# Kernel tuning notes

Hardware: AMD Instinct MI355X
Metric: run time of the kernel (lower is better)

## Reference

```python
import jax, jax.numpy as jnp
import numpy as np

N, E, G = 30000, 480000, 64
IN, H, L = 24, 512, 6


def setup_inputs() -> dict:
    key = jax.random.key(0)
    ks = jax.random.split(key, 20)
    s = 0.05
    inp = {
        "x": jax.random.normal(ks[0], (N, IN), dtype=jnp.float32),
        "edge_index": jax.random.randint(ks[1], (2, E), 0, N, dtype=jnp.int64),
        "batch": jnp.sort(jax.random.randint(ks[2], (N,), 0, G, dtype=jnp.int64)),
        # node encoder
        "enc_w": jax.random.normal(ks[3], (IN, H), dtype=jnp.float32) * s,
        "enc_b": jnp.zeros((H,), dtype=jnp.float32),
        # per-layer message MLP (stacked over L layers), weights stored [in, out]
        "mlp_w1": jax.random.normal(ks[4], (L, H, H), dtype=jnp.float32) * s,
        "mlp_b1": jnp.zeros((L, H), dtype=jnp.float32),
        "mlp_w2": jax.random.normal(ks[5], (L, H, H), dtype=jnp.float32) * s,
        "mlp_b2": jnp.zeros((L, H), dtype=jnp.float32),
        # per-layer GRUCell params, [in, 3H] layout (gates order: r, z, n)
        "gru_wih": jax.random.normal(ks[6], (L, H, 3 * H), dtype=jnp.float32) * s,
        "gru_whh": jax.random.normal(ks[7], (L, H, 3 * H), dtype=jnp.float32) * s,
        "gru_bih": jnp.zeros((L, 3 * H), dtype=jnp.float32),
        "gru_bhh": jnp.zeros((L, 3 * H), dtype=jnp.float32),
        # head MLP
        "head_w1": jax.random.normal(ks[8], (H, H // 2), dtype=jnp.float32) * s,
        "head_b1": jnp.zeros((H // 2,), dtype=jnp.float32),
        "head_w2": jax.random.normal(ks[9], (H // 2, 1), dtype=jnp.float32) * s,
        "head_b2": jnp.zeros((1,), dtype=jnp.float32),
    }
    return inp


def _forward(x, edge_index, batch, enc_w, enc_b, mlp_w1, mlp_b1, mlp_w2, mlp_b2,
             gru_wih, gru_whh, gru_bih, gru_bhh, head_w1, head_b1, head_w2, head_b2):
    src, dst = edge_index[0], edge_index[1]
    h = x @ enc_w + enc_b  # [N, H]
    for l in range(L):
        # message MLP depends only on x_j, so compute per-node then gather
        msg = jnp.maximum(h @ mlp_w1[l] + mlp_b1[l], 0.0) @ mlp_w2[l] + mlp_b2[l]  # [N, H]
        # scatter-add over edges + self-loop contribution (add_self_loops)
        m = jax.ops.segment_sum(msg[src], dst, num_segments=N) + msg  # [N, H]
        # GRUCell(input=m, hidden=h); torch gate order: reset, update, new
        gi = m @ gru_wih[l] + gru_bih[l]
        gh = h @ gru_whh[l] + gru_bhh[l]
        r = jax.nn.sigmoid(gi[:, :H] + gh[:, :H])
        z = jax.nn.sigmoid(gi[:, H:2 * H] + gh[:, H:2 * H])
        n = jnp.tanh(gi[:, 2 * H:] + r * gh[:, 2 * H:])
        h = (1.0 - z) * n + z * h
    # global mean pool per graph
    sums = jax.ops.segment_sum(h, batch, num_segments=G)
    cnt = jax.ops.segment_sum(jnp.ones((N,), dtype=h.dtype), batch, num_segments=G)
    pooled = sums / jnp.maximum(cnt, 1.0)[:, None]  # [G, H]
    out = jnp.maximum(pooled @ head_w1 + head_b1, 0.0) @ head_w2 + head_b2
    return out[:, 0]  # [G]


def reference(x, edge_index, batch, enc_w, enc_b, mlp_w1, mlp_b1, mlp_w2, mlp_b2,
              gru_wih, gru_whh, gru_bih, gru_bhh, head_w1, head_b1, head_w2, head_b2):
    return _forward(x, edge_index, batch, enc_w, enc_b, mlp_w1, mlp_b1, mlp_w2, mlp_b2,
                    gru_wih, gru_whh, gru_bih, gru_bhh, head_w1, head_b1, head_w2, head_b2)
```

## Files before the change

kernel.cpp:

```cpp
#include <hip/hip_runtime.h>
#include <hip/hip_bf16.h>
#include <math.h>

#define N_NODES 30000
#define N_EDGES 480000
#define N_GRAPH 64
#define DIN 24
#define HD 512
#define NL 6

typedef __hip_bfloat16 bf16;
using short8 = __attribute__((ext_vector_type(8))) short;
using f32x4 = __attribute__((ext_vector_type(4))) float;

#define ASYNC16(gp, lp)                                              \
    __builtin_amdgcn_global_load_lds(                                \
        (const __attribute__((address_space(1))) void*)(gp),         \
        (__attribute__((address_space(3))) void*)(lp), 16, 0, 0)

__device__ __forceinline__ float sigmoidf_(float x) { return 1.0f / (1.0f + expf(-x)); }
__device__ __forceinline__ float b2f(unsigned short u) {
    return __uint_as_float(((unsigned int)u) << 16);
}
__device__ __forceinline__ unsigned short f2b(float f) {
    bf16 b = __float2bfloat16(f);
    return *(unsigned short*)&b;
}

__global__ __launch_bounds__(256) void enc_kernel(const float* __restrict__ x,
                                                  const float* __restrict__ w,
                                                  const float* __restrict__ b,
                                                  bf16* __restrict__ h) {
    __shared__ float xs[DIN];
    int row = blockIdx.x;
    int tid = threadIdx.x;
    if (tid < DIN) xs[tid] = x[row * DIN + tid];
    __syncthreads();
    for (int c = tid; c < HD; c += 256) {
        float acc = b[c];
#pragma unroll
        for (int k = 0; k < DIN; k++) acc = fmaf(xs[k], w[k * HD + c], acc);
        h[(size_t)row * HD + c] = __float2bfloat16(acc);
    }
}

__global__ __launch_bounds__(256) void twcvt_kernel(const float* __restrict__ W,
                                                    bf16* __restrict__ WtH,
                                                    bf16* __restrict__ WtL, int Nc) {
    __shared__ float s[32][33];
    int l = blockIdx.z;
    const float* Wp = W + (size_t)l * HD * Nc;
    size_t ob = (size_t)l * HD * Nc;
    int k0 = blockIdx.y * 32, c0 = blockIdx.x * 32;
    int tx = threadIdx.x & 31, ty = threadIdx.x >> 5;
    for (int r = ty; r < 32; r += 8) s[r][tx] = Wp[(size_t)(k0 + r) * Nc + c0 + tx];
    __syncthreads();
    for (int r = ty; r < 32; r += 8) {
        float v = s[tx][r];
        unsigned short hu = f2b(v);
        float hf = b2f(hu);
        size_t o = ob + (size_t)(c0 + r) * HD + k0 + tx;
        *(unsigned short*)&WtH[o] = hu;
        WtL[o] = __float2bfloat16(v - hf);
    }
}

template <bool RELU>
__global__ __launch_bounds__(256) void gemm_mfma(const bf16* __restrict__ A,
                                                 const bf16* __restrict__ WtH,
                                                 const bf16* __restrict__ WtL,
                                                 const float* __restrict__ bias,
                                                 bf16* __restrict__ C, int n) {
    __shared__ bf16 As[128 * 32];
    __shared__ bf16 BH[128 * 32];
    __shared__ bf16 BL[128 * 32];
    int tid = threadIdx.x;
    int wv = tid >> 6, lane = tid & 63;
    int quad = lane >> 4, l16 = lane & 15;
    int crow = lane >> 2, cseg = lane & 3;
    int gseg = cseg ^ ((crow >> 1) & 3);
    int fsw = (quad ^ ((l16 >> 1) & 3)) * 8;
    int row0 = blockIdx.y * 128, col0 = blockIdx.x * 128;
    f32x4 acc[2][8] = {};

    int aoff[4], alds[4];
    int boff[8];
    const bf16* wb = (wv == 2) ? WtH : WtL;
    bf16* bdst = (wv == 2) ? BH : BL;
    if (wv < 2) {
#pragma unroll
        for (int j = 0; j < 4; j++) {
            int ch = wv * 4 + j;
            int gr = row0 + ch * 16 + crow;
            if (gr > n - 1) gr = n - 1;
            aoff[j] = gr * HD + gseg * 8;
            alds[j] = ch * 512;
        }
    } else {
#pragma unroll
        for (int s = 0; s < 8; s++) boff[s] = (col0 + s * 16 + crow) * HD + gseg * 8;
    }

    for (int kt = 0; kt < 512; kt += 32) {
        if (wv < 2) {
#pragma unroll
            for (int j = 0; j < 4; j++) ASYNC16(&A[aoff[j] + kt], &As[alds[j]]);
        } else {
#pragma unroll
            for (int s = 0; s < 8; s++) ASYNC16(&wb[boff[s] + kt], &bdst[s * 512]);
        }
        __syncthreads();
        short8 bfr[2][2];
#pragma unroll
        for (int t = 0; t < 2; t++) {
            int fo = ((wv * 2 + t) * 16 + l16) * 32 + fsw;
            bfr[t][0] = *(const short8*)&BH[fo];
            bfr[t][1] = *(const short8*)&BL[fo];
        }
#pragma unroll
        for (int i = 0; i < 8; i++) {
            short8 af = *(const short8*)&As[(i * 16 + l16) * 32 + fsw];
#pragma unroll
            for (int t = 0; t < 2; t++) {
                acc[t][i] = __builtin_amdgcn_mfma_f32_16x16x32_bf16(af, bfr[t][0], acc[t][i], 0, 0, 0);
                acc[t][i] = __builtin_amdgcn_mfma_f32_16x16x32_bf16(af, bfr[t][1], acc[t][i], 0, 0, 0);
            }
        }
        __syncthreads();
    }
#pragma unroll
    for (int t = 0; t < 2; t++) {
        int col = col0 + (wv * 2 + t) * 16 + l16;
        float bb = bias[col];
#pragma unroll
        for (int i = 0; i < 8; i++) {
#pragma unroll
            for (int r = 0; r < 4; r++) {
                int row = row0 + i * 16 + quad * 4 + r;
                if (row < n) {
                    float v = acc[t][i][r] + bb;
                    if (RELU) v = fmaxf(v, 0.0f);
                    C[(size_t)row * HD + col] = __float2bfloat16(v);
                }
            }
        }
    }
}

__global__ __launch_bounds__(256, 2) void gru_mfma(const bf16* __restrict__ M,
                                                   const bf16* __restrict__ Hc,
                                                   const bf16* __restrict__ WiH,
                                                   const bf16* __restrict__ WiL,
                                                   const bf16* __restrict__ WhH,
                                                   const bf16* __restrict__ WhL,
                                                   const float* __restrict__ bih,
                                                   const float* __restrict__ bhh,
                                                   bf16* __restrict__ Hn, int n) {
    __shared__ bf16 Ms[128 * 32];
    __shared__ bf16 Hs[128 * 32];
    __shared__ bf16 Ws[12 * 64 * 32];
    int tid = threadIdx.x;
    int wv = tid >> 6, lane = tid & 63;
    int quad = lane >> 4, l16 = lane & 15;
    int crow = lane >> 2, cseg = lane & 3;
    int gseg = cseg ^ ((crow >> 1) & 3);
    int fsw = (quad ^ ((l16 >> 1) & 3)) * 8;
    int row0 = blockIdx.y * 128, col0 = blockIdx.x * 64;
    f32x4 aR[8] = {}, aZ[8] = {}, aI[8] = {}, aHn[8] = {};

    int moff[8];
    const bf16* wgp[4];
    int wlds[4];
    if (wv == 0) {
#pragma unroll
        for (int j = 0; j < 8; j++) {
            int gr = row0 + j * 16 + crow;
            if (gr > n - 1) gr = n - 1;
            moff[j] = gr * HD + gseg * 8;
        }
    } else {
        const bf16* wbase[4] = {WiH, WiL, WhH, WhL};
#pragma unroll
        for (int pp = 0; pp < 4; pp++) {
            int p = (wv - 1) * 4 + pp;
            int mat = (p >= 6);
            int q = p - mat * 6;
            int g = q >> 1, pl = q & 1;
            const bf16* base = wbase[mat * 2 + pl] + (size_t)(g * HD + col0) * HD;
            wgp[pp] = base + crow * HD + gseg * 8;
            wlds[pp] = p * 2048;
        }
    }

    for (int kt = 0; kt < 512; kt += 32) {
        if (wv == 0) {
#pragma unroll
            for (int j = 0; j < 8; j++) {
                ASYNC16(&M[moff[j] + kt], &Ms[j * 512]);
                ASYNC16(&Hc[moff[j] + kt], &Hs[j * 512]);
            }
        } else {
#pragma unroll
            for (int pp = 0; pp < 4; pp++)
#pragma unroll
                for (int s = 0; s < 4; s++)
                    ASYNC16(wgp[pp] + (size_t)s * 16 * HD + kt, &Ws[wlds[pp] + s * 512]);
        }
        __syncthreads();
        int fo = (wv * 16 + l16) * 32 + fsw;
        short8 wrh = *(const short8*)&Ws[0 * 2048 + fo];
        short8 wrl = *(const short8*)&Ws[1 * 2048 + fo];
        short8 wzh = *(const short8*)&Ws[2 * 2048 + fo];
        short8 wzl = *(const short8*)&Ws[3 * 2048 + fo];
        short8 wnh = *(const short8*)&Ws[4 * 2048 + fo];
        short8 wnl = *(const short8*)&Ws[5 * 2048 + fo];
        short8 vrh = *(const short8*)&Ws[6 * 2048 + fo];
        short8 vrl = *(const short8*)&Ws[7 * 2048 + fo];
        short8 vzh = *(const short8*)&Ws[8 * 2048 + fo];
        short8 vzl = *(const short8*)&Ws[9 * 2048 + fo];
        short8 vnh = *(const short8*)&Ws[10 * 2048 + fo];
        short8 vnl = *(const short8*)&Ws[11 * 2048 + fo];
#pragma unroll
        for (int i = 0; i < 8; i++) {
            short8 am = *(const short8*)&Ms[(i * 16 + l16) * 32 + fsw];
            short8 ah = *(const short8*)&Hs[(i * 16 + l16) * 32 + fsw];
            aR[i] = __builtin_amdgcn_mfma_f32_16x16x32_bf16(am, wrh, aR[i], 0, 0, 0);
            aR[i] = __builtin_amdgcn_mfma_f32_16x16x32_bf16(am, wrl, aR[i], 0, 0, 0);
            aR[i] = __builtin_amdgcn_mfma_f32_16x16x32_bf16(ah, vrh, aR[i], 0, 0, 0);
            aR[i] = __builtin_amdgcn_mfma_f32_16x16x32_bf16(ah, vrl, aR[i], 0, 0, 0);
            aZ[i] = __builtin_amdgcn_mfma_f32_16x16x32_bf16(am, wzh, aZ[i], 0, 0, 0);
            aZ[i] = __builtin_amdgcn_mfma_f32_16x16x32_bf16(am, wzl, aZ[i], 0, 0, 0);
            aZ[i] = __builtin_amdgcn_mfma_f32_16x16x32_bf16(ah, vzh, aZ[i], 0, 0, 0);
            aZ[i] = __builtin_amdgcn_mfma_f32_16x16x32_bf16(ah, vzl, aZ[i], 0, 0, 0);
            aI[i] = __builtin_amdgcn_mfma_f32_16x16x32_bf16(am, wnh, aI[i], 0, 0, 0);
            aI[i] = __builtin_amdgcn_mfma_f32_16x16x32_bf16(am, wnl, aI[i], 0, 0, 0);
            aHn[i] = __builtin_amdgcn_mfma_f32_16x16x32_bf16(ah, vnh, aHn[i], 0, 0, 0);
            aHn[i] = __builtin_amdgcn_mfma_f32_16x16x32_bf16(ah, vnl, aHn[i], 0, 0, 0);
        }
        __syncthreads();
    }
    const unsigned short* hp = (const unsigned short*)Hc;
    int col = col0 + wv * 16 + l16;
    float brz = bih[col] + bhh[col];
    float bzz = bih[HD + col] + bhh[HD + col];
    float bin_ = bih[2 * HD + col];
    float bhn_ = bhh[2 * HD + col];
#pragma unroll
    for (int i = 0; i < 8; i++) {
#pragma unroll
        for (int r = 0; r < 4; r++) {
            int row = row0 + i * 16 + quad * 4 + r;
            if (row < n) {
                float rg = sigmoidf_(aR[i][r] + brz);
                float zg = sigmoidf_(aZ[i][r] + bzz);
                float ng = tanhf(aI[i][r] + bin_ + rg * (aHn[i][r] + bhn_));
                float hold = b2f(hp[(size_t)row * HD + col]);
                Hn[(size_t)row * HD + col] = __float2bfloat16((1.0f - zg) * ng + zg * hold);
            }
        }
    }
}

__global__ __launch_bounds__(256) void deg_kernel(const int* __restrict__ dst,
                                                  int* __restrict__ deg) {
    int e = blockIdx.x * 256 + threadIdx.x;
    if (e < N_EDGES) atomicAdd(&deg[dst[e]], 1);
}

__global__ __launch_bounds__(1024) void scan_kernel(const int* __restrict__ deg,
                                                    int* __restrict__ offs) {
    __shared__ int buf[1024];
    __shared__ int carry_s;
    int tid = threadIdx.x;
    if (tid == 0) carry_s = 0;
    __syncthreads();
    for (int base = 0; base < N_NODES; base += 1024) {
        int v = (base + tid < N_NODES) ? deg[base + tid] : 0;
        buf[tid] = v;
        __syncthreads();
        for (int s = 1; s < 1024; s <<= 1) {
            int t = (tid >= s) ? buf[tid - s] : 0;
            __syncthreads();
            buf[tid] += t;
            __syncthreads();
        }
        int incl = buf[tid];
        if (base + tid < N_NODES) offs[base + tid] = carry_s + incl - v;
        __syncthreads();
        if (tid == 0) carry_s += buf[1023];
        __syncthreads();
    }
    if (tid == 0) offs[N_NODES] = carry_s;
}

__global__ __launch_bounds__(256) void bucket_kernel(const int* __restrict__ src,
                                                     const int* __restrict__ dst,
                                                     const int* __restrict__ offs,
                                                     int* __restrict__ cursor,
                                                     unsigned short* __restrict__ elist) {
    int e = blockIdx.x * 256 + threadIdx.x;
    if (e >= N_EDGES) return;
    int d = dst[e];
    int pos = atomicAdd(&cursor[d], 1);
    elist[offs[d] + pos] = (unsigned short)src[e];
}

__global__ __launch_bounds__(256) void gather_kernel(const bf16* __restrict__ msg,
                                                     bf16* __restrict__ m,
                                                     const unsigned short* __restrict__ elist,
                                                     const int* __restrict__ offs) {
    int nid = blockIdx.x, tid = threadIdx.x;
    int beg = offs[nid], end = offs[nid + 1];
    const unsigned int* mp = (const unsigned int*)msg;
    unsigned int u = mp[(size_t)nid * 256 + tid];
    float ax = b2f((unsigned short)(u & 0xffffu));
    float ay = b2f((unsigned short)(u >> 16));
    int e = beg;
    for (; e + 3 < end; e += 4) {
        unsigned int v0 = mp[(size_t)elist[e] * 256 + tid];
        unsigned int v1 = mp[(size_t)elist[e + 1] * 256 + tid];
        unsigned int v2 = mp[(size_t)elist[e + 2] * 256 + tid];
        unsigned int v3 = mp[(size_t)elist[e + 3] * 256 + tid];
        ax += b2f((unsigned short)(v0 & 0xffffu)) + b2f((unsigned short)(v1 & 0xffffu)) +
              b2f((unsigned short)(v2 & 0xffffu)) + b2f((unsigned short)(v3 & 0xffffu));
        ay += b2f((unsigned short)(v0 >> 16)) + b2f((unsigned short)(v1 >> 16)) +
              b2f((unsigned short)(v2 >> 16)) + b2f((unsigned short)(v3 >> 16));
    }
    for (; e < end; e++) {
        unsigned int v0 = mp[(size_t)elist[e] * 256 + tid];
        ax += b2f((unsigned short)(v0 & 0xffffu));
        ay += b2f((unsigned short)(v0 >> 16));
    }
    unsigned int out = ((unsigned int)f2b(ay) << 16) | (unsigned int)f2b(ax);
    ((unsigned int*)m)[(size_t)nid * 256 + tid] = out;
}

__global__ __launch_bounds__(256) void pool_kernel(const bf16* __restrict__ h,
                                                   const int* __restrict__ batch,
                                                   float* __restrict__ pooled,
                                                   float* __restrict__ cnt) {
    int g = blockIdx.x;
    int col = blockIdx.y * 256 + threadIdx.x;
    int lo = 0, hi = N_NODES;
    while (lo < hi) { int mid = (lo + hi) >> 1; if (batch[mid] < g) lo = mid + 1; else hi = mid; }
    int gs = lo;
    hi = N_NODES;
    while (lo < hi) { int mid = (lo + hi) >> 1; if (batch[mid] < g + 1) lo = mid + 1; else hi = mid; }
    int ge = lo;
    const unsigned short* hp = (const unsigned short*)h;
    float acc = 0.0f;
    int r = gs;
    for (; r + 3 < ge; r += 4) {
        acc += b2f(hp[(size_t)r * HD + col]) + b2f(hp[(size_t)(r + 1) * HD + col]) +
               b2f(hp[(size_t)(r + 2) * HD + col]) + b2f(hp[(size_t)(r + 3) * HD + col]);
    }
    for (; r < ge; r++) acc += b2f(hp[(size_t)r * HD + col]);
    pooled[g * HD + col] = acc;
    if (blockIdx.y == 0 && threadIdx.x == 0) cnt[g] = (float)(ge - gs);
}

__global__ __launch_bounds__(256) void head_kernel(const float* __restrict__ pooled,
                                                   const float* __restrict__ cnt,
                                                   const float* __restrict__ w1,
                                                   const float* __restrict__ b1,
                                                   const float* __restrict__ w2,
                                                   const float* __restrict__ b2,
                                                   float* __restrict__ out) {
    __shared__ float prow[HD];
    __shared__ float red[256];
    int g = blockIdx.x, tid = threadIdx.x;
    float c = fmaxf(cnt[g], 1.0f);
    for (int j = tid; j < HD; j += 256) prow[j] = pooled[g * HD + j] / c;
    __syncthreads();
    float acc = b1[tid];
    for (int k = 0; k < HD; k++) acc = fmaf(prow[k], w1[k * 256 + tid], acc);
    red[tid] = fmaxf(acc, 0.0f) * w2[tid];
    __syncthreads();
    for (int s = 128; s > 0; s >>= 1) {
        if (tid < s) red[tid] += red[tid + s];
        __syncthreads();
    }
    if (tid == 0) out[g] = red[0] + b2[0];
}

extern "C" void kernel_launch(void* const* d_in, const int* in_sizes, int n_in,
                              void* d_out, int out_size, void* d_ws, size_t ws_size,
                              hipStream_t stream) {
    const float* x = (const float*)d_in[0];
    const int* eidx = (const int*)d_in[1];
    const int* batch = (const int*)d_in[2];
    const float* enc_w = (const float*)d_in[3];
    const float* enc_b = (const float*)d_in[4];
    const float* mlp_w1 = (const float*)d_in[5];
    const float* mlp_b1 = (const float*)d_in[6];
    const float* mlp_w2 = (const float*)d_in[7];
    const float* mlp_b2 = (const float*)d_in[8];
    const float* gru_wih = (const float*)d_in[9];
    const float* gru_whh = (const float*)d_in[10];
    const float* gru_bih = (const float*)d_in[11];
    const float* gru_bhh = (const float*)d_in[12];
    const float* head_w1 = (const float*)d_in[13];
    const float* head_b1 = (const float*)d_in[14];
    const float* head_w2 = (const float*)d_in[15];
    const float* head_b2 = (const float*)d_in[16];
    const int* src = eidx;
    const int* dst = eidx + N_EDGES;

    const size_t NH = (size_t)N_NODES * HD;
    char* p = (char*)d_ws;
    auto alloc = [&](size_t bytes) { char* q = p; p += (bytes + 255) & ~(size_t)255; return q; };
    bf16* S0 = (bf16*)alloc(NH * 2);
    bf16* S1 = (bf16*)alloc(NH * 2);
    bf16* S2 = (bf16*)alloc(NH * 2);
    bf16* w1tH = (bf16*)alloc((size_t)NL * HD * HD * 2);
    bf16* w1tL = (bf16*)alloc((size_t)NL * HD * HD * 2);
    bf16* w2tH = (bf16*)alloc((size_t)NL * HD * HD * 2);
    bf16* w2tL = (bf16*)alloc((size_t)NL * HD * HD * 2);
    bf16* wihtH = (bf16*)alloc((size_t)NL * 3 * HD * HD * 2);
    bf16* wihtL = (bf16*)alloc((size_t)NL * 3 * HD * HD * 2);
    bf16* whhtH = (bf16*)alloc((size_t)NL * 3 * HD * HD * 2);
    bf16* whhtL = (bf16*)alloc((size_t)NL * 3 * HD * HD * 2);
    float* pooled = (float*)alloc((size_t)N_GRAPH * HD * 4);
    float* cnt = (float*)alloc(N_GRAPH * 4);
    int* deg = (int*)alloc((N_NODES + 1) * 4);
    int* offs = (int*)alloc((N_NODES + 1) * 4);
    unsigned short* elist = (unsigned short*)alloc((size_t)N_EDGES * 2);

    twcvt_kernel<<<dim3(16, 16, NL), 256, 0, stream>>>(mlp_w1, w1tH, w1tL, HD);
    twcvt_kernel<<<dim3(16, 16, NL), 256, 0, stream>>>(mlp_w2, w2tH, w2tL, HD);
    twcvt_kernel<<<dim3(48, 16, NL), 256, 0, stream>>>(gru_wih, wihtH, wihtL, 3 * HD);
    twcvt_kernel<<<dim3(48, 16, NL), 256, 0, stream>>>(gru_whh, whhtH, whhtL, 3 * HD);

    hipMemsetAsync(deg, 0, (N_NODES + 1) * sizeof(int), stream);
    deg_kernel<<<(N_EDGES + 255) / 256, 256, 0, stream>>>(dst, deg);
    scan_kernel<<<1, 1024, 0, stream>>>(deg, offs);
    hipMemsetAsync(deg, 0, (N_NODES + 1) * sizeof(int), stream);
    bucket_kernel<<<(N_EDGES + 255) / 256, 256, 0, stream>>>(src, dst, offs, deg, elist);

    enc_kernel<<<N_NODES, 256, 0, stream>>>(x, enc_w, enc_b, S0);

    bf16* hcur = S0;
    bf16* hoth = S1;
    dim3 ggrid(4, (N_NODES + 127) / 128);
    dim3 ugrid(8, (N_NODES + 127) / 128);

    for (int l = 0; l < NL; l++) {
        size_t wsq = (size_t)l * HD * HD;
        size_t wgq = (size_t)l * 3 * HD * HD;
        const float* b1 = mlp_b1 + (size_t)l * HD;
        const float* b2 = mlp_b2 + (size_t)l * HD;
        const float* bih = gru_bih + (size_t)l * 3 * HD;
        const float* bhh = gru_bhh + (size_t)l * 3 * HD;

        gemm_mfma<true><<<ggrid, 256, 0, stream>>>(hcur, w1tH + wsq, w1tL + wsq, b1, hoth, N_NODES);
        gemm_mfma<false><<<ggrid, 256, 0, stream>>>(hoth, w2tH + wsq, w2tL + wsq, b2, S2, N_NODES);
        gather_kernel<<<N_NODES, 256, 0, stream>>>(S2, hoth, elist, offs);
        gru_mfma<<<ugrid, 256, 0, stream>>>(hoth, hcur, wihtH + wgq, wihtL + wgq,
                                            whhtH + wgq, whhtL + wgq, bih, bhh, S2, N_NODES);
        bf16* newh = S2;
        S2 = hcur;
        hcur = newh;
    }

    pool_kernel<<<dim3(N_GRAPH, 2), 256, 0, stream>>>(hcur, batch, pooled, cnt);
    head_kernel<<<N_GRAPH, 256, 0, stream>>>(pooled, cnt, head_w1, head_b1, head_w2, head_b2,
                                             (float*)d_out);
}
```

Baseline: 2.854 ms.

## Overlap next K-tile async loads with MFMA in MLP and GRU GEMM loops

Restructures the K loops of the MLP GEMM and the fused GRU GEMM so the next K slice's global-to-LDS loads are issued right after the current slice's fragments are read into registers. This lets the loads overlap the MFMA work instead of sitting behind a full barrier. The GRU kernel splits the activation staging into two halves so each half is refilled as soon as it has been consumed. Explicit vmcnt/lgkmcnt waits with raw barriers and setprio around the MFMA blocks are added. It keeps a single LDS buffer, so correctness depends on the waits being placed exactly right, and register pressure goes up from holding the fragments.

```diff
diff --git a/kernel.cpp b/kernel.cpp
--- a/kernel.cpp
+++ b/kernel.cpp
@@ -17,6 +17,19 @@
     __builtin_amdgcn_global_load_lds(                                \
         (const __attribute__((address_space(1))) void*)(gp),         \
         (__attribute__((address_space(3))) void*)(lp), 16, 0, 0)
+
+#define WAIT_VM0_BAR()                                               \
+    do {                                                             \
+        asm volatile("s_waitcnt vmcnt(0)" ::: "memory");             \
+        __builtin_amdgcn_sched_barrier(0);                           \
+        __builtin_amdgcn_s_barrier();                                \
+    } while (0)
+#define WAIT_LGKM0_BAR()                                             \
+    do {                                                             \
+        asm volatile("s_waitcnt lgkmcnt(0)" ::: "memory");           \
+        __builtin_amdgcn_sched_barrier(0);                           \
+        __builtin_amdgcn_s_barrier();                                \
+    } while (0)
 
 __device__ __forceinline__ float sigmoidf_(float x) { return 1.0f / (1.0f + expf(-x)); }
 __device__ __forceinline__ float b2f(unsigned short u) {
@@ -101,7 +114,7 @@
         for (int s = 0; s < 8; s++) boff[s] = (col0 + s * 16 + crow) * HD + gseg * 8;
     }
 
-    for (int kt = 0; kt < 512; kt += 32) {
+    auto stage = [&](int kt) {
         if (wv < 2) {
 #pragma unroll
             for (int j = 0; j < 4; j++) ASYNC16(&A[aoff[j] + kt], &As[alds[j]]);
@@ -109,7 +122,11 @@
 #pragma unroll
             for (int s = 0; s < 8; s++) ASYNC16(&wb[boff[s] + kt], &bdst[s * 512]);
         }
-        __syncthreads();
+    };
+
+    stage(0);
+    for (int kt = 0; kt < 512; kt += 32) {
+        WAIT_VM0_BAR();
         short8 bfr[2][2];
 #pragma unroll
         for (int t = 0; t < 2; t++) {
@@ -117,16 +134,21 @@
             bfr[t][0] = *(const short8*)&BH[fo];
             bfr[t][1] = *(const short8*)&BL[fo];
         }
+        short8 af[8];
+#pragma unroll
+        for (int i = 0; i < 8; i++) af[i] = *(const short8*)&As[(i * 16 + l16) * 32 + fsw];
+        WAIT_LGKM0_BAR();
+        if (kt + 32 < 512) stage(kt + 32);
+        __builtin_amdgcn_s_setprio(1);
 #pragma unroll
         for (int i = 0; i < 8; i++) {
-            short8 af = *(const short8*)&As[(i * 16 + l16) * 32 + fsw];
 #pragma unroll
             for (int t = 0; t < 2; t++) {
-                acc[t][i] = __builtin_amdgcn_mfma_f32_16x16x32_bf16(af, bfr[t][0], acc[t][i], 0, 0, 0);
-                acc[t][i] = __builtin_amdgcn_mfma_f32_16x16x32_bf16(af, bfr[t][1], acc[t][i], 0, 0, 0);
+                acc[t][i] = __builtin_amdgcn_mfma_f32_16x16x32_bf16(af[i], bfr[t][0], acc[t][i], 0, 0, 0);
+                acc[t][i] = __builtin_amdgcn_mfma_f32_16x16x32_bf16(af[i], bfr[t][1], acc[t][i], 0, 0, 0);
             }
         }
-        __syncthreads();
+        __builtin_amdgcn_s_setprio(0);
     }
 #pragma unroll
     for (int t = 0; t < 2; t++) {
@@ -192,10 +214,10 @@
         }
     }
 
-    for (int kt = 0; kt < 512; kt += 32) {
+    auto stage1 = [&](int kt) {
         if (wv == 0) {
 #pragma unroll
-            for (int j = 0; j < 8; j++) {
+            for (int j = 0; j < 4; j++) {
                 ASYNC16(&M[moff[j] + kt], &Ms[j * 512]);
                 ASYNC16(&Hc[moff[j] + kt], &Hs[j * 512]);
             }
@@ -206,7 +228,21 @@
                 for (int s = 0; s < 4; s++)
                     ASYNC16(wgp[pp] + (size_t)s * 16 * HD + kt, &Ws[wlds[pp] + s * 512]);
         }
-        __syncthreads();
+    };
+    auto stage2 = [&](int kt) {
+        if (wv == 0) {
+#pragma unroll
+            for (int j = 4; j < 8; j++) {
+                ASYNC16(&M[moff[j] + kt], &Ms[j * 512]);
+                ASYNC16(&Hc[moff[j] + kt], &Hs[j * 512]);
+            }
+        }
+    };
+
+    stage1(0);
+    stage2(0);
+    for (int kt = 0; kt < 512; kt += 32) {
+        WAIT_VM0_BAR();
         int fo = (wv * 16 + l16) * 32 + fsw;
         short8 wrh = *(const short8*)&Ws[0 * 2048 + fo];
         short8 wrl = *(const short8*)&Ws[1 * 2048 + fo];
@@ -220,24 +256,57 @@
         short8 vzl = *(const short8*)&Ws[9 * 2048 + fo];
         short8 vnh = *(const short8*)&Ws[10 * 2048 + fo];
         short8 vnl = *(const short8*)&Ws[11 * 2048 + fo];
-#pragma unroll
-        for (int i = 0; i < 8; i++) {
-            short8 am = *(const short8*)&Ms[(i * 16 + l16) * 32 + fsw];
-            short8 ah = *(const short8*)&Hs[(i * 16 + l16) * 32 + fsw];
-            aR[i] = __builtin_amdgcn_mfma_f32_16x16x32_bf16(am, wrh, aR[i], 0, 0, 0);
-            aR[i] = __builtin_amdgcn_mfma_f32_16x16x32_bf16(am, wrl, aR[i], 0, 0, 0);
-            aR[i] = __builtin_amdgcn_mfma_f32_16x16x32_bf16(ah, vrh, aR[i], 0, 0, 0);
-            aR[i] = __builtin_amdgcn_mfma_f32_16x16x32_bf16(ah, vrl, aR[i], 0, 0, 0);
-            aZ[i] = __builtin_amdgcn_mfma_f32_16x16x32_bf16(am, wzh, aZ[i], 0, 0, 0);
-            aZ[i] = __builtin_amdgcn_mfma_f32_16x16x32_bf16(am, wzl, aZ[i], 0, 0, 0);
-            aZ[i] = __builtin_amdgcn_mfma_f32_16x16x32_bf16(ah, vzh, aZ[i], 0, 0, 0);
-            aZ[i] = __builtin_amdgcn_mfma_f32_16x16x32_bf16(ah, vzl, aZ[i], 0, 0, 0);
-            aI[i] = __builtin_amdgcn_mfma_f32_16x16x32_bf16(am, wnh, aI[i], 0, 0, 0);
-            aI[i] = __builtin_amdgcn_mfma_f32_16x16x32_bf16(am, wnl, aI[i], 0, 0, 0);
-            aHn[i] = __builtin_amdgcn_mfma_f32_16x16x32_bf16(ah, vnh, aHn[i], 0, 0, 0);
-            aHn[i] = __builtin_amdgcn_mfma_f32_16x16x32_bf16(ah, vnl, aHn[i], 0, 0, 0);
-        }
-        __syncthreads();
+        short8 am[4], ah[4];
+#pragma unroll
+        for (int i = 0; i < 4; i++) {
+            am[i] = *(const short8*)&Ms[(i * 16 + l16) * 32 + fsw];
+            ah[i] = *(const short8*)&Hs[(i * 16 + l16) * 32 + fsw];
+        }
+        WAIT_LGKM0_BAR();
+        bool more = (kt + 32 < 512);
+        if (more) stage1(kt + 32);
+        __builtin_amdgcn_s_setprio(1);
+#pragma unroll
+        for (int i = 0; i < 4; i++) {
+            aR[i] = __builtin_amdgcn_mfma_f32_16x16x32_bf16(am[i], wrh, aR[i], 0, 0, 0);
+            aR[i] = __builtin_amdgcn_mfma_f32_16x16x32_bf16(am[i], wrl, aR[i], 0, 0, 0);
+            aR[i] = __builtin_amdgcn_mfma_f32_16x16x32_bf16(ah[i], vrh, aR[i], 0, 0, 0);
+            aR[i] = __builtin_amdgcn_mfma_f32_16x16x32_bf16(ah[i], vrl, aR[i], 0, 0, 0);
+            aZ[i] = __builtin_amdgcn_mfma_f32_16x16x32_bf16(am[i], wzh, aZ[i], 0, 0, 0);
+            aZ[i] = __builtin_amdgcn_mfma_f32_16x16x32_bf16(am[i], wzl, aZ[i], 0, 0, 0);
+            aZ[i] = __builtin_amdgcn_mfma_f32_16x16x32_bf16(ah[i], vzh, aZ[i], 0, 0, 0);
+            aZ[i] = __builtin_amdgcn_mfma_f32_16x16x32_bf16(ah[i], vzl, aZ[i], 0, 0, 0);
+            aI[i] = __builtin_amdgcn_mfma_f32_16x16x32_bf16(am[i], wnh, aI[i], 0, 0, 0);
+            aI[i] = __builtin_amdgcn_mfma_f32_16x16x32_bf16(am[i], wnl, aI[i], 0, 0, 0);
+            aHn[i] = __builtin_amdgcn_mfma_f32_16x16x32_bf16(ah[i], vnh, aHn[i], 0, 0, 0);
+            aHn[i] = __builtin_amdgcn_mfma_f32_16x16x32_bf16(ah[i], vnl, aHn[i], 0, 0, 0);
+        }
+        __builtin_amdgcn_s_setprio(0);
+        short8 bm[4], bh_[4];
+#pragma unroll
+        for (int i = 0; i < 4; i++) {
+            bm[i] = *(const short8*)&Ms[((i + 4) * 16 + l16) * 32 + fsw];
+            bh_[i] = *(const short8*)&Hs[((i + 4) * 16 + l16) * 32 + fsw];
+        }
+        WAIT_LGKM0_BAR();
+        if (more) stage2(kt + 32);
+        __builtin_amdgcn_s_setprio(1);
+#pragma unroll
+        for (int i = 0; i < 4; i++) {
+            aR[i + 4] = __builtin_amdgcn_mfma_f32_16x16x32_bf16(bm[i], wrh, aR[i + 4], 0, 0, 0);
+            aR[i + 4] = __builtin_amdgcn_mfma_f32_16x16x32_bf16(bm[i], wrl, aR[i + 4], 0, 0, 0);
+            aR[i + 4] = __builtin_amdgcn_mfma_f32_16x16x32_bf16(bh_[i], vrh, aR[i + 4], 0, 0, 0);
+            aR[i + 4] = __builtin_amdgcn_mfma_f32_16x16x32_bf16(bh_[i], vrl, aR[i + 4], 0, 0, 0);
+            aZ[i + 4] = __builtin_amdgcn_mfma_f32_16x16x32_bf16(bm[i], wzh, aZ[i + 4], 0, 0, 0);
+            aZ[i + 4] = __builtin_amdgcn_mfma_f32_16x16x32_bf16(bm[i], wzl, aZ[i + 4], 0, 0, 0);
+            aZ[i + 4] = __builtin_amdgcn_mfma_f32_16x16x32_bf16(bh_[i], vzh, aZ[i + 4], 0, 0, 0);
+            aZ[i + 4] = __builtin_amdgcn_mfma_f32_16x16x32_bf16(bh_[i], vzl, aZ[i + 4], 0, 0, 0);
+            aI[i + 4] = __builtin_amdgcn_mfma_f32_16x16x32_bf16(bm[i], wnh, aI[i + 4], 0, 0, 0);
+            aI[i + 4] = __builtin_amdgcn_mfma_f32_16x16x32_bf16(bm[i], wnl, aI[i + 4], 0, 0, 0);
+            aHn[i + 4] = __builtin_amdgcn_mfma_f32_16x16x32_bf16(bh_[i], vnh, aHn[i + 4], 0, 0, 0);
+            aHn[i + 4] = __builtin_amdgcn_mfma_f32_16x16x32_bf16(bh_[i], vnl, aHn[i + 4], 0, 0, 0);
+        }
+        __builtin_amdgcn_s_setprio(0);
     }
     const unsigned short* hp = (const unsigned short*)Hc;
     int col = col0 + wv * 16 + l16;
```

After: 2.923 ms. +2.4%, slower.

## Double-buffer LDS tiles and spread async loads across all waves in GEMM/GRU

Applied to the files above, without the earlier changes.

The MLP GEMM and GRU kernels now double-buffer their activation tiles in LDS and prefetch the next K-slice while the current one is consumed. The GEMM replaces two barriers per iteration with one explicit waitcnt plus barrier, and the GRU single-buffers its weights behind a second barrier. Loads are now issued by every wave instead of dedicated loader waves, and MFMA sections raise wave priority. The aim is to hide global-to-LDS latency behind MFMA work, at the cost of more LDS use per block and an occupancy hint of 3 on the GEMM.

```diff
diff --git a/kernel.cpp b/kernel.cpp
--- a/kernel.cpp
+++ b/kernel.cpp
@@ -17,6 +17,19 @@
     __builtin_amdgcn_global_load_lds(                                \
         (const __attribute__((address_space(1))) void*)(gp),         \
         (__attribute__((address_space(3))) void*)(lp), 16, 0, 0)
+
+#define WAITALL_BAR()                                                \
+    do {                                                             \
+        asm volatile("s_waitcnt vmcnt(0) lgkmcnt(0)" ::: "memory");  \
+        __builtin_amdgcn_sched_barrier(0);                           \
+        __builtin_amdgcn_s_barrier();                                \
+    } while (0)
+#define LGKM_BAR()                                                   \
+    do {                                                             \
+        asm volatile("s_waitcnt lgkmcnt(0)" ::: "memory");           \
+        __builtin_amdgcn_sched_barrier(0);                           \
+        __builtin_amdgcn_s_barrier();                                \
+    } while (0)
 
 __device__ __forceinline__ float sigmoidf_(float x) { return 1.0f / (1.0f + expf(-x)); }
 __device__ __forceinline__ float b2f(unsigned short u) {
@@ -66,14 +79,12 @@
 }
 
 template <bool RELU>
-__global__ __launch_bounds__(256) void gemm_mfma(const bf16* __restrict__ A,
-                                                 const bf16* __restrict__ WtH,
-                                                 const bf16* __restrict__ WtL,
-                                                 const float* __restrict__ bias,
-                                                 bf16* __restrict__ C, int n) {
-    __shared__ bf16 As[128 * 32];
-    __shared__ bf16 BH[128 * 32];
-    __shared__ bf16 BL[128 * 32];
+__global__ __launch_bounds__(256, 3) void gemm_mfma(const bf16* __restrict__ A,
+                                                    const bf16* __restrict__ WtH,
+                                                    const bf16* __restrict__ WtL,
+                                                    const float* __restrict__ bias,
+                                                    bf16* __restrict__ C, int n) {
+    __shared__ bf16 SB[2][3 * 128 * 32];
     int tid = threadIdx.x;
     int wv = tid >> 6, lane = tid & 63;
     int quad = lane >> 4, l16 = lane & 15;
@@ -83,50 +94,48 @@
     int row0 = blockIdx.y * 128, col0 = blockIdx.x * 128;
     f32x4 acc[2][8] = {};
 
-    int aoff[4], alds[4];
-    int boff[8];
-    const bf16* wb = (wv == 2) ? WtH : WtL;
-    bf16* bdst = (wv == 2) ? BH : BL;
-    if (wv < 2) {
-#pragma unroll
-        for (int j = 0; j < 4; j++) {
-            int ch = wv * 4 + j;
-            int gr = row0 + ch * 16 + crow;
+    const bf16* gsrc[6];
+#pragma unroll
+    for (int j = 0; j < 6; j++) {
+        int c = wv * 6 + j;
+        if (c < 8) {
+            int gr = row0 + c * 16 + crow;
             if (gr > n - 1) gr = n - 1;
-            aoff[j] = gr * HD + gseg * 8;
-            alds[j] = ch * 512;
-        }
-    } else {
-#pragma unroll
-        for (int s = 0; s < 8; s++) boff[s] = (col0 + s * 16 + crow) * HD + gseg * 8;
-    }
-
-    for (int kt = 0; kt < 512; kt += 32) {
-        if (wv < 2) {
-#pragma unroll
-            for (int j = 0; j < 4; j++) ASYNC16(&A[aoff[j] + kt], &As[alds[j]]);
+            gsrc[j] = A + (size_t)gr * HD + gseg * 8;
+        } else if (c < 16) {
+            gsrc[j] = WtH + (size_t)(col0 + (c - 8) * 16 + crow) * HD + gseg * 8;
         } else {
-#pragma unroll
-            for (int s = 0; s < 8; s++) ASYNC16(&wb[boff[s] + kt], &bdst[s * 512]);
-        }
-        __syncthreads();
+            gsrc[j] = WtL + (size_t)(col0 + (c - 16) * 16 + crow) * HD + gseg * 8;
+        }
+    }
+    auto stage = [&](int kt, int nb) {
+#pragma unroll
+        for (int j = 0; j < 6; j++) ASYNC16(gsrc[j] + kt, &SB[nb][(wv * 6 + j) * 512]);
+    };
+
+    stage(0, 0);
+    for (int t16 = 0; t16 < 16; t16++) {
+        int b = t16 & 1;
+        WAITALL_BAR();
+        if (t16 < 15) stage((t16 + 1) * 32, b ^ 1);
         short8 bfr[2][2];
 #pragma unroll
         for (int t = 0; t < 2; t++) {
             int fo = ((wv * 2 + t) * 16 + l16) * 32 + fsw;
-            bfr[t][0] = *(const short8*)&BH[fo];
-            bfr[t][1] = *(const short8*)&BL[fo];
-        }
+            bfr[t][0] = *(const short8*)&SB[b][4096 + fo];
+            bfr[t][1] = *(const short8*)&SB[b][8192 + fo];
+        }
+        __builtin_amdgcn_s_setprio(1);
 #pragma unroll
         for (int i = 0; i < 8; i++) {
-            short8 af = *(const short8*)&As[(i * 16 + l16) * 32 + fsw];
+            short8 af = *(const short8*)&SB[b][(i * 16 + l16) * 32 + fsw];
 #pragma unroll
             for (int t = 0; t < 2; t++) {
                 acc[t][i] = __builtin_amdgcn_mfma_f32_16x16x32_bf16(af, bfr[t][0], acc[t][i], 0, 0, 0);
                 acc[t][i] = __builtin_amdgcn_mfma_f32_16x16x32_bf16(af, bfr[t][1], acc[t][i], 0, 0, 0);
             }
         }
-        __syncthreads();
+        __builtin_amdgcn_s_setprio(0);
     }
 #pragma unroll
     for (int t = 0; t < 2; t++) {
@@ -156,8 +165,7 @@
                                                    const float* __restrict__ bih,
                                                    const float* __restrict__ bhh,
                                                    bf16* __restrict__ Hn, int n) {
-    __shared__ bf16 Ms[128 * 32];
-    __shared__ bf16 Hs[128 * 32];
+    __shared__ bf16 MH[2][2 * 128 * 32];
     __shared__ bf16 Ws[12 * 64 * 32];
     int tid = threadIdx.x;
     int wv = tid >> 6, lane = tid & 63;
@@ -168,46 +176,46 @@
     int row0 = blockIdx.y * 128, col0 = blockIdx.x * 64;
     f32x4 aR[8] = {}, aZ[8] = {}, aI[8] = {}, aHn[8] = {};
 
-    int moff[8];
-    const bf16* wgp[4];
-    int wlds[4];
-    if (wv == 0) {
-#pragma unroll
-        for (int j = 0; j < 8; j++) {
-            int gr = row0 + j * 16 + crow;
-            if (gr > n - 1) gr = n - 1;
-            moff[j] = gr * HD + gseg * 8;
-        }
-    } else {
-        const bf16* wbase[4] = {WiH, WiL, WhH, WhL};
-#pragma unroll
-        for (int pp = 0; pp < 4; pp++) {
-            int p = (wv - 1) * 4 + pp;
-            int mat = (p >= 6);
-            int q = p - mat * 6;
-            int g = q >> 1, pl = q & 1;
-            const bf16* base = wbase[mat * 2 + pl] + (size_t)(g * HD + col0) * HD;
-            wgp[pp] = base + crow * HD + gseg * 8;
-            wlds[pp] = p * 2048;
-        }
-    }
-
-    for (int kt = 0; kt < 512; kt += 32) {
-        if (wv == 0) {
-#pragma unroll
-            for (int j = 0; j < 8; j++) {
-                ASYNC16(&M[moff[j] + kt], &Ms[j * 512]);
-                ASYNC16(&Hc[moff[j] + kt], &Hs[j * 512]);
-            }
-        } else {
-#pragma unroll
-            for (int pp = 0; pp < 4; pp++)
-#pragma unroll
-                for (int s = 0; s < 4; s++)
-                    ASYNC16(wgp[pp] + (size_t)s * 16 * HD + kt, &Ws[wlds[pp] + s * 512]);
-        }
-        __syncthreads();
-        int fo = (wv * 16 + l16) * 32 + fsw;
+    const bf16* mhsrc[4];
+#pragma unroll
+    for (int j = 0; j < 4; j++) {
+        int c = wv * 4 + j;
+        int gr = row0 + (c & 7) * 16 + crow;
+        if (gr > n - 1) gr = n - 1;
+        mhsrc[j] = (c < 8 ? M : Hc) + (size_t)gr * HD + gseg * 8;
+    }
+    const bf16* wbase[4] = {WiH, WiL, WhH, WhL};
+    const bf16* wgp[3];
+#pragma unroll
+    for (int pp = 0; pp < 3; pp++) {
+        int p = wv * 3 + pp;
+        int mat = (p >= 6);
+        int q = p - mat * 6;
+        int g = q >> 1, pl = q & 1;
+        const bf16* base = wbase[mat * 2 + pl] + (size_t)(g * HD + col0) * HD;
+        wgp[pp] = base + crow * HD + gseg * 8;
+    }
+    auto stageMH = [&](int kt, int nb) {
+#pragma unroll
+        for (int j = 0; j < 4; j++) ASYNC16(mhsrc[j] + kt, &MH[nb][(wv * 4 + j) * 512]);
+    };
+    auto stageW = [&](int kt) {
+#pragma unroll
+        for (int pp = 0; pp < 3; pp++)
+#pragma unroll
+            for (int s = 0; s < 4; s++)
+                ASYNC16(wgp[pp] + (size_t)s * 16 * HD + kt, &Ws[(wv * 3 + pp) * 2048 + s * 512]);
+    };
+
+    stageMH(0, 0);
+    stageW(0);
+    int fo = (wv * 16 + l16) * 32 + fsw;
+    for (int t16 = 0; t16 < 16; t16++) {
+        int b = t16 & 1;
+        int kt = t16 * 32;
+        bool more = (t16 < 15);
+        WAITALL_BAR();
+        if (more) stageMH(kt + 32, b ^ 1);
         short8 wrh = *(const short8*)&Ws[0 * 2048 + fo];
         short8 wrl = *(const short8*)&Ws[1 * 2048 + fo];
         short8 wzh = *(const short8*)&Ws[2 * 2048 + fo];
@@ -220,10 +228,13 @@
         short8 vzl = *(const short8*)&Ws[9 * 2048 + fo];
         short8 vnh = *(const short8*)&Ws[10 * 2048 + fo];
         short8 vnl = *(const short8*)&Ws[11 * 2048 + fo];
+        LGKM_BAR();
+        if (more) stageW(kt + 32);
+        __builtin_amdgcn_s_setprio(1);
 #pragma unroll
         for (int i = 0; i < 8; i++) {
-            short8 am = *(const short8*)&Ms[(i * 16 + l16) * 32 + fsw];
-            short8 ah = *(const short8*)&Hs[(i * 16 + l16) * 32 + fsw];
+            short8 am = *(const short8*)&MH[b][(i * 16 + l16) * 32 + fsw];
+            short8 ah = *(const short8*)&MH[b][4096 + (i * 16 + l16) * 32 + fsw];
             aR[i] = __builtin_amdgcn_mfma_f32_16x16x32_bf16(am, wrh, aR[i], 0, 0, 0);
             aR[i] = __builtin_amdgcn_mfma_f32_16x16x32_bf16(am, wrl, aR[i], 0, 0, 0);
             aR[i] = __builtin_amdgcn_mfma_f32_16x16x32_bf16(ah, vrh, aR[i], 0, 0, 0);
@@ -237,7 +248,7 @@
             aHn[i] = __builtin_amdgcn_mfma_f32_16x16x32_bf16(ah, vnh, aHn[i], 0, 0, 0);
             aHn[i] = __builtin_amdgcn_mfma_f32_16x16x32_bf16(ah, vnl, aHn[i], 0, 0, 0);
         }
-        __syncthreads();
+        __builtin_amdgcn_s_setprio(0);
     }
     const unsigned short* hp = (const unsigned short*)Hc;
     int col = col0 + wv * 16 + l16;
```

After: 2.851 ms. Within noise of the previous version (-0.1%).

## Double-buffer GEMM LDS loads and stage epilogues through LDS for coalesced stores

Applied to the files above, without the earlier changes.

The message-MLP GEMM now double-buffers its A and weight tiles in one LDS array, issuing the next k-tile's async loads before computing the current one. It spreads loading evenly across all four waves, raises MFMA priority, and sets occupancy to three blocks per CU. Both the GEMM and GRU epilogues now stage results in LDS and write 16-byte coalesced rows instead of scattered 2-byte stores. The GRU also reads the old hidden state with vector loads. This aims to hide global load latency and cut uncoalesced store traffic, at the cost of more LDS per block and extra barriers.

```diff
diff --git a/kernel.cpp b/kernel.cpp
--- a/kernel.cpp
+++ b/kernel.cpp
@@ -17,6 +17,13 @@
     __builtin_amdgcn_global_load_lds(                                \
         (const __attribute__((address_space(1))) void*)(gp),         \
         (__attribute__((address_space(3))) void*)(lp), 16, 0, 0)
+
+#define WAITALL_BAR()                                                \
+    do {                                                             \
+        asm volatile("s_waitcnt vmcnt(0) lgkmcnt(0)" ::: "memory");  \
+        __builtin_amdgcn_sched_barrier(0);                           \
+        __builtin_amdgcn_s_barrier();                                \
+    } while (0)
 
 __device__ __forceinline__ float sigmoidf_(float x) { return 1.0f / (1.0f + expf(-x)); }
 __device__ __forceinline__ float b2f(unsigned short u) {
@@ -66,14 +73,12 @@
 }
 
 template <bool RELU>
-__global__ __launch_bounds__(256) void gemm_mfma(const bf16* __restrict__ A,
-                                                 const bf16* __restrict__ WtH,
-                                                 const bf16* __restrict__ WtL,
-                                                 const float* __restrict__ bias,
-                                                 bf16* __restrict__ C, int n) {
-    __shared__ bf16 As[128 * 32];
-    __shared__ bf16 BH[128 * 32];
-    __shared__ bf16 BL[128 * 32];
+__global__ __launch_bounds__(256, 3) void gemm_mfma(const bf16* __restrict__ A,
+                                                    const bf16* __restrict__ WtH,
+                                                    const bf16* __restrict__ WtL,
+                                                    const float* __restrict__ bias,
+                                                    bf16* __restrict__ C, int n) {
+    __shared__ __align__(16) bf16 SB[2][3 * 128 * 32];
     int tid = threadIdx.x;
     int wv = tid >> 6, lane = tid & 63;
     int quad = lane >> 4, l16 = lane & 15;
@@ -83,66 +88,82 @@
     int row0 = blockIdx.y * 128, col0 = blockIdx.x * 128;
     f32x4 acc[2][8] = {};
 
-    int aoff[4], alds[4];
-    int boff[8];
-    const bf16* wb = (wv == 2) ? WtH : WtL;
-    bf16* bdst = (wv == 2) ? BH : BL;
-    if (wv < 2) {
-#pragma unroll
-        for (int j = 0; j < 4; j++) {
-            int ch = wv * 4 + j;
-            int gr = row0 + ch * 16 + crow;
+    const bf16* gsrc[6];
+#pragma unroll
+    for (int j = 0; j < 6; j++) {
+        int c = wv * 6 + j;
+        if (c < 8) {
+            int gr = row0 + c * 16 + crow;
             if (gr > n - 1) gr = n - 1;
-            aoff[j] = gr * HD + gseg * 8;
-            alds[j] = ch * 512;
-        }
-    } else {
-#pragma unroll
-        for (int s = 0; s < 8; s++) boff[s] = (col0 + s * 16 + crow) * HD + gseg * 8;
-    }
-
-    for (int kt = 0; kt < 512; kt += 32) {
-        if (wv < 2) {
-#pragma unroll
-            for (int j = 0; j < 4; j++) ASYNC16(&A[aoff[j] + kt], &As[alds[j]]);
+            gsrc[j] = A + (size_t)gr * HD + gseg * 8;
+        } else if (c < 16) {
+            gsrc[j] = WtH + (size_t)(col0 + (c - 8) * 16 + crow) * HD + gseg * 8;
         } else {
-#pragma unroll
-            for (int s = 0; s < 8; s++) ASYNC16(&wb[boff[s] + kt], &bdst[s * 512]);
-        }
-        __syncthreads();
+            gsrc[j] = WtL + (size_t)(col0 + (c - 16) * 16 + crow) * HD + gseg * 8;
+        }
+    }
+    auto stage = [&](int kt, int nb) {
+#pragma unroll
+        for (int j = 0; j < 6; j++) ASYNC16(gsrc[j] + kt, &SB[nb][(wv * 6 + j) * 512]);
+    };
+
+    stage(0, 0);
+    for (int t16 = 0; t16 < 16; t16++) {
+        int b = t16 & 1;
+        WAITALL_BAR();
+        if (t16 < 15) stage((t16 + 1) * 32, b ^ 1);
         short8 bfr[2][2];
 #pragma unroll
         for (int t = 0; t < 2; t++) {
             int fo = ((wv * 2 + t) * 16 + l16) * 32 + fsw;
-            bfr[t][0] = *(const short8*)&BH[fo];
-            bfr[t][1] = *(const short8*)&BL[fo];
-        }
+            bfr[t][0] = *(const short8*)&SB[b][4096 + fo];
+            bfr[t][1] = *(const short8*)&SB[b][8192 + fo];
+        }
+        __builtin_amdgcn_s_setprio(1);
 #pragma unroll
         for (int i = 0; i < 8; i++) {
-            short8 af = *(const short8*)&As[(i * 16 + l16) * 32 + fsw];
+            short8 af = *(const short8*)&SB[b][(i * 16 + l16) * 32 + fsw];
 #pragma unroll
             for (int t = 0; t < 2; t++) {
                 acc[t][i] = __builtin_amdgcn_mfma_f32_16x16x32_bf16(af, bfr[t][0], acc[t][i], 0, 0, 0);
                 acc[t][i] = __builtin_amdgcn_mfma_f32_16x16x32_bf16(af, bfr[t][1], acc[t][i], 0, 0, 0);
             }
         }
-        __syncthreads();
-    }
+        __builtin_amdgcn_s_setprio(0);
+    }
+    __syncthreads();
+    bf16* Cs = (bf16*)SB;
 #pragma unroll
     for (int t = 0; t < 2; t++) {
-        int col = col0 + (wv * 2 + t) * 16 + l16;
-        float bb = bias[col];
+        int colL = (wv * 2 + t) * 16 + l16;
+        float bb = bias[col0 + colL];
 #pragma unroll
         for (int i = 0; i < 8; i++) {
 #pragma unroll
             for (int r = 0; r < 4; r++) {
-                int row = row0 + i * 16 + quad * 4 + r;
-                if (row < n) {
-                    float v = acc[t][i][r] + bb;
-                    if (RELU) v = fmaxf(v, 0.0f);
-                    C[(size_t)row * HD + col] = __float2bfloat16(v);
-                }
+                int rowL = i * 16 + quad * 4 + r;
+                float v = acc[t][i][r] + bb;
+                if (RELU) v = fmaxf(v, 0.0f);
+                Cs[rowL * 132 + colL] = __float2bfloat16(v);
             }
+        }
+    }
+    __syncthreads();
+    const unsigned short* cp = (const unsigned short*)Cs;
+#pragma unroll
+    for (int pass = 0; pass < 8; pass++) {
+        int rowL = pass * 16 + (tid >> 4);
+        int row = row0 + rowL;
+        int cc = (tid & 15) * 8;
+        if (row < n) {
+            ushort4 a0 = *(const ushort4*)&cp[rowL * 132 + cc];
+            ushort4 a1 = *(const ushort4*)&cp[rowL * 132 + cc + 4];
+            uint4 ov;
+            ov.x = ((unsigned int)a0.y << 16) | a0.x;
+            ov.y = ((unsigned int)a0.w << 16) | a0.z;
+            ov.z = ((unsigned int)a1.y << 16) | a1.x;
+            ov.w = ((unsigned int)a1.w << 16) | a1.z;
+            *(uint4*)&((unsigned short*)C)[(size_t)row * HD + col0 + cc] = ov;
         }
     }
 }
@@ -156,9 +177,9 @@
                                                    const float* __restrict__ bih,
                                                    const float* __restrict__ bhh,
                                                    bf16* __restrict__ Hn, int n) {
-    __shared__ bf16 Ms[128 * 32];
-    __shared__ bf16 Hs[128 * 32];
-    __shared__ bf16 Ws[12 * 64 * 32];
+    __shared__ __align__(16) bf16 Ms[128 * 32];
+    __shared__ __align__(16) bf16 Hs[128 * 32];
+    __shared__ __align__(16) bf16 Ws[12 * 64 * 32];
     int tid = threadIdx.x;
     int wv = tid >> 6, lane = tid & 63;
     int quad = lane >> 4, l16 = lane & 15;
@@ -192,6 +213,7 @@
         }
     }
 
+    int fo = (wv * 16 + l16) * 32 + fsw;
     for (int kt = 0; kt < 512; kt += 32) {
         if (wv == 0) {
 #pragma unroll
@@ -207,7 +229,6 @@
                     ASYNC16(wgp[pp] + (size_t)s * 16 * HD + kt, &Ws[wlds[pp] + s * 512]);
         }
         __syncthreads();
-        int fo = (wv * 16 + l16) * 32 + fsw;
         short8 wrh = *(const short8*)&Ws[0 * 2048 + fo];
         short8 wrl = *(const short8*)&Ws[1 * 2048 + fo];
         short8 wzh = *(const short8*)&Ws[2 * 2048 + fo];
@@ -239,25 +260,58 @@
         }
         __syncthreads();
     }
-    const unsigned short* hp = (const unsigned short*)Hc;
-    int col = col0 + wv * 16 + l16;
+    float* Zs32 = (float*)Ws;
+    float* Ps32 = Zs32 + 64 * 66;
+    int colL = wv * 16 + l16;
+    int col = col0 + colL;
     float brz = bih[col] + bhh[col];
     float bzz = bih[HD + col] + bhh[HD + col];
     float bin_ = bih[2 * HD + col];
     float bhn_ = bhh[2 * HD + col];
-#pragma unroll
-    for (int i = 0; i < 8; i++) {
-#pragma unroll
-        for (int r = 0; r < 4; r++) {
-            int row = row0 + i * 16 + quad * 4 + r;
+    const unsigned short* hp = (const unsigned short*)Hc;
+    unsigned short* op = (unsigned short*)Hn;
+#pragma unroll
+    for (int hhalf = 0; hhalf < 2; hhalf++) {
+#pragma unroll
+        for (int i = 0; i < 4; i++) {
+            int ii = hhalf * 4 + i;
+#pragma unroll
+            for (int r = 0; r < 4; r++) {
+                int rowL = i * 16 + quad * 4 + r;
+                float rg = sigmoidf_(aR[ii][r] + brz);
+                float zg = sigmoidf_(aZ[ii][r] + bzz);
+                float ng = tanhf(aI[ii][r] + bin_ + rg * (aHn[ii][r] + bhn_));
+                Zs32[rowL * 66 + colL] = zg;
+                Ps32[rowL * 66 + colL] = (1.0f - zg) * ng;
+            }
+        }
+        __syncthreads();
+#pragma unroll
+        for (int sub = 0; sub < 2; sub++) {
+            int rowL = sub * 32 + (tid >> 3);
+            int row = row0 + hhalf * 64 + rowL;
+            int cc = (tid & 7) * 8;
             if (row < n) {
-                float rg = sigmoidf_(aR[i][r] + brz);
-                float zg = sigmoidf_(aZ[i][r] + bzz);
-                float ng = tanhf(aI[i][r] + bin_ + rg * (aHn[i][r] + bhn_));
-                float hold = b2f(hp[(size_t)row * HD + col]);
-                Hn[(size_t)row * HD + col] = __float2bfloat16((1.0f - zg) * ng + zg * hold);
+                uint4 hv = *(const uint4*)&hp[(size_t)row * HD + col0 + cc];
+                unsigned int hw[4] = {hv.x, hv.y, hv.z, hv.w};
+                unsigned int ow[4];
+#pragma unroll
+                for (int q = 0; q < 4; q++) {
+                    float h0 = b2f((unsigned short)(hw[q] & 0xffffu));
+                    float h1 = b2f((unsigned short)(hw[q] >> 16));
+                    float z0 = Zs32[rowL * 66 + cc + 2 * q];
+                    float z1 = Zs32[rowL * 66 + cc + 2 * q + 1];
+                    float p0 = Ps32[rowL * 66 + cc + 2 * q];
+                    float p1 = Ps32[rowL * 66 + cc + 2 * q + 1];
+                    float o0 = fmaf(z0, h0, p0);
+                    float o1 = fmaf(z1, h1, p1);
+                    ow[q] = ((unsigned int)f2b(o1) << 16) | f2b(o0);
+                }
+                uint4 ov = {ow[0], ow[1], ow[2], ow[3]};
+                *(uint4*)&op[(size_t)row * HD + col0 + cc] = ov;
             }
         }
+        __syncthreads();
     }
 }
 
```

New measurement: 2.525 ms. 11.5% less time.
